# Optimization experiments

Hardware: AMD Instinct MI355X
Metric: run time of the kernel (lower is better)

The kernel has to match this reference:

```python
import jax, jax.numpy as jnp
import numpy as np

N = 8192        # num_nodes (also num output classes per the module)
F_IN = 512      # num_features
H = 64          # gcn_dim
E = N * 64      # edges (avg_degree 64)


def setup_inputs() -> dict:
    key = jax.random.key(0)
    k_x, k_e, k_w1, k_w2 = jax.random.split(key, 4)
    x = jax.random.normal(k_x, (N, F_IN), dtype=jnp.float32)
    edge_index = jax.random.randint(k_e, (2, E), 0, N, dtype=jnp.int64)
    # Glorot-ish init for the two GCN layer weights
    W1 = jax.random.normal(k_w1, (F_IN, H), dtype=jnp.float32) * (1.0 / np.sqrt(F_IN))
    b1 = jnp.zeros((H,), dtype=jnp.float32)
    W2 = jax.random.normal(k_w2, (H, N), dtype=jnp.float32) * (1.0 / np.sqrt(H))
    b2 = jnp.zeros((N,), dtype=jnp.float32)
    return {"x": x, "edge_index": edge_index, "W1": W1, "b1": b1, "W2": W2, "b2": b2}


def _gcn_conv(x, edge_index, W, b):
    """GCNConv: out = D^{-1/2} (A + I) D^{-1/2} (x @ W) + b."""
    n = x.shape[0]
    loops = jnp.arange(n, dtype=edge_index.dtype)
    src = jnp.concatenate([edge_index[0], loops])  # message source nodes
    dst = jnp.concatenate([edge_index[1], loops])  # aggregation targets
    deg = jax.ops.segment_sum(jnp.ones_like(dst, dtype=x.dtype), dst, num_segments=n)
    dinv = jnp.where(deg > 0, jax.lax.rsqrt(deg), 0.0)
    norm = dinv[src] * dinv[dst]                   # [E+n]
    xw = x @ W                                     # transform first (smaller msgs when W shrinks dim)
    msgs = xw[src] * norm[:, None]                 # gather + scale
    return jax.ops.segment_sum(msgs, dst, num_segments=n) + b


def reference(x, edge_index, W1, b1, W2, b2):
    h = jax.nn.relu(_gcn_conv(x, edge_index, W1, b1))   # [N, H]
    logits = _gcn_conv(h, edge_index, W2, b2)           # [N, N]
    return jax.nn.log_softmax(logits, axis=1)
```

## Files before the change

kernel.cpp:

```cpp
#include <hip/hip_runtime.h>
#include <hip/hip_bf16.h>

typedef __attribute__((ext_vector_type(8))) short short8;
typedef __attribute__((ext_vector_type(16))) float f32x16;
typedef __attribute__((ext_vector_type(4))) float f32x4;

#define NN 8192
#define FIN 512
#define HD 64
#define LOG2E 1.44269504088896f

#if __has_builtin(__builtin_amdgcn_exp2f)
#define EXP2(x) __builtin_amdgcn_exp2f(x)
#else
#define EXP2(x) exp2f(x)
#endif

__global__ void k_pack_zero(const float* __restrict__ W2, __hip_bfloat16* __restrict__ w2p,
                            int* __restrict__ cnt) {
    int i = blockIdx.x * blockDim.x + threadIdx.x;
    if (i < NN) cnt[i] = 0;
    int k  = i >> 13;
    int cc = i & 8191;
    int c32 = cc >> 5, cl = cc & 31;
    int kc = k >> 4, hh = (k >> 3) & 1, j = k & 7;
    int dsti = ((c32 * 4 + kc) * 64 + hh * 32 + cl) * 8 + j;
    w2p[dsti] = __float2bfloat16(W2[i]);
}

__global__ void k_count(const int* __restrict__ dst, int E, int* __restrict__ cnt) {
    int e = blockIdx.x * blockDim.x + threadIdx.x;
    if (e < E) atomicAdd(&cnt[dst[e]], 1);
}

__global__ __launch_bounds__(1024) void k_scan(const int* __restrict__ cnt,
        int* __restrict__ offs, int* __restrict__ cursor, float* __restrict__ dinv) {
    __shared__ int wsh[16];
    int t = threadIdx.x;
    int lane = t & 63, wv = t >> 6;
    int v[8], loc[8];
    int s = 0;
#pragma unroll
    for (int j = 0; j < 8; ++j) { v[j] = cnt[t*8+j]; loc[j] = s; s += v[j]; }
    int inc = s;
#pragma unroll
    for (int d = 1; d < 64; d <<= 1) {
        int up = __shfl_up(inc, d, 64);
        if (lane >= d) inc += up;
    }
    if (lane == 63) wsh[wv] = inc;
    __syncthreads();
    if (t < 16) {
        int mv = wsh[t];
        int winc = mv;
#pragma unroll
        for (int d = 1; d < 16; d <<= 1) {
            int up = __shfl_up(winc, d, 16);
            if (t >= d) winc += up;
        }
        wsh[t] = winc - mv;
    }
    __syncthreads();
    int base = wsh[wv] + (inc - s);
#pragma unroll
    for (int j = 0; j < 8; ++j) {
        int o = base + loc[j];
        offs[t*8+j]   = o;
        cursor[t*8+j] = o;
        dinv[t*8+j]   = rsqrtf((float)(v[j] + 1));
    }
    if (t == 1023) offs[NN] = base + s;
}

__global__ void k_scatter(const int* __restrict__ src, const int* __restrict__ dst, int E,
        int* __restrict__ cursor, int* __restrict__ ssrc) {
    int e = blockIdx.x * blockDim.x + threadIdx.x;
    if (e < E) {
        int pos = atomicAdd(&cursor[dst[e]], 1);
        ssrc[pos] = src[e];
    }
}

__global__ __launch_bounds__(256) void k_gemm1(const float* __restrict__ x,
        const float* __restrict__ W1, const float* __restrict__ dinv,
        float* __restrict__ xws) {
    __shared__ alignas(16) float Xs[16][132];
    int t = threadIdx.x;
    int c  = t & 63;
    int rg = t >> 6;
    int br = blockIdx.x * 16;
    float acc[4] = {0.f, 0.f, 0.f, 0.f};
    for (int k0 = 0; k0 < FIN; k0 += 128) {
        __syncthreads();
        int row_ld = t >> 4, kcol = (t & 15) * 8;
        const float* xp = x + (br + row_ld) * FIN + k0 + kcol;
        float4 v0 = *(const float4*)xp;
        float4 v1 = *(const float4*)(xp + 4);
        *(float4*)&Xs[row_ld][kcol]     = v0;
        *(float4*)&Xs[row_ld][kcol + 4] = v1;
        __syncthreads();
        int rg4 = rg * 4;
#pragma unroll 4
        for (int kk = 0; kk < 128; kk += 4) {
            f32x4 x0 = *(const f32x4*)&Xs[rg4 + 0][kk];
            f32x4 x1 = *(const f32x4*)&Xs[rg4 + 1][kk];
            f32x4 x2 = *(const f32x4*)&Xs[rg4 + 2][kk];
            f32x4 x3 = *(const f32x4*)&Xs[rg4 + 3][kk];
#pragma unroll
            for (int q = 0; q < 4; ++q) {
                float w = W1[(k0 + kk + q) * HD + c];
                acc[0] += x0[q] * w;
                acc[1] += x1[q] * w;
                acc[2] += x2[q] * w;
                acc[3] += x3[q] * w;
            }
        }
    }
#pragma unroll
    for (int r = 0; r < 4; ++r) {
        int row = br + rg*4 + r;
        xws[row * HD + c] = acc[r] * dinv[row];
    }
}

__global__ __launch_bounds__(256) void k_agg1(const float* __restrict__ xws,
        const int* __restrict__ offs, const int* __restrict__ ssrc,
        const float* __restrict__ dinv, const float* __restrict__ b1,
        float* __restrict__ hs) {
    int lane = threadIdx.x & 63;
    int node = (blockIdx.x << 2) + (threadIdx.x >> 6);
    const float* xp = xws + lane;
    float acc = xp[node * HD];
    int beg = offs[node], end = offs[node + 1];
    for (int base = beg; base < end; base += 64) {
        int rem = end - base;
        int n = rem < 64 ? rem : 64;
        int idx = (lane < n) ? ssrc[base + lane] : 0;
        int j = 0;
        for (; j + 8 <= n; j += 8) {
            int s0 = __shfl(idx, j+0, 64), s1 = __shfl(idx, j+1, 64);
            int s2 = __shfl(idx, j+2, 64), s3 = __shfl(idx, j+3, 64);
            int s4 = __shfl(idx, j+4, 64), s5 = __shfl(idx, j+5, 64);
            int s6 = __shfl(idx, j+6, 64), s7 = __shfl(idx, j+7, 64);
            float v0 = xp[s0*HD], v1 = xp[s1*HD], v2 = xp[s2*HD], v3 = xp[s3*HD];
            float v4 = xp[s4*HD], v5 = xp[s5*HD], v6 = xp[s6*HD], v7 = xp[s7*HD];
            acc += ((v0+v1)+(v2+v3)) + ((v4+v5)+(v6+v7));
        }
        for (; j < n; ++j) {
            int s = __shfl(idx, j, 64);
            acc += xp[s*HD];
        }
    }
    float dv = dinv[node];
    float h = fmaxf(acc * dv + b1[lane], 0.f);
    hs[node * HD + lane] = h * dv;
}

__global__ __launch_bounds__(256) void k_agg2(const float* __restrict__ hs,
        const int* __restrict__ offs, const int* __restrict__ ssrc,
        const float* __restrict__ dinv, __hip_bfloat16* __restrict__ gbf) {
    int lane = threadIdx.x & 63;
    int node = (blockIdx.x << 2) + (threadIdx.x >> 6);
    const float* hp = hs + lane;
    float acc = hp[node * HD];
    int beg = offs[node], end = offs[node + 1];
    for (int base = beg; base < end; base += 64) {
        int rem = end - base;
        int n = rem < 64 ? rem : 64;
        int idx = (lane < n) ? ssrc[base + lane] : 0;
        int j = 0;
        for (; j + 8 <= n; j += 8) {
            int s0 = __shfl(idx, j+0, 64), s1 = __shfl(idx, j+1, 64);
            int s2 = __shfl(idx, j+2, 64), s3 = __shfl(idx, j+3, 64);
            int s4 = __shfl(idx, j+4, 64), s5 = __shfl(idx, j+5, 64);
            int s6 = __shfl(idx, j+6, 64), s7 = __shfl(idx, j+7, 64);
            float v0 = hp[s0*HD], v1 = hp[s1*HD], v2 = hp[s2*HD], v3 = hp[s3*HD];
            float v4 = hp[s4*HD], v5 = hp[s5*HD], v6 = hp[s6*HD], v7 = hp[s7*HD];
            acc += ((v0+v1)+(v2+v3)) + ((v4+v5)+(v6+v7));
        }
        for (; j < n; ++j) {
            int s = __shfl(idx, j, 64);
            acc += hp[s*HD];
        }
    }
    gbf[node * HD + lane] = __float2bfloat16(acc * dinv[node]);
}

__global__ __launch_bounds__(512) void k_fused(
        const __hip_bfloat16* __restrict__ gbf,
        const __hip_bfloat16* __restrict__ w2p,
        const float* __restrict__ b2,
        float* __restrict__ out) {
    __shared__ float red[32][8];
    __shared__ float Lsh[32];
    const unsigned short* g  = (const unsigned short*)gbf;
    const unsigned short* wp = (const unsigned short*)w2p;
    int t = threadIdx.x;
    int lane = t & 63, wv = t >> 6;
    int cl = lane & 31, hh = lane >> 5;
    int row0 = blockIdx.x * 32;

    short8 a[4];
#pragma unroll
    for (int kc = 0; kc < 4; ++kc)
        a[kc] = *(const short8*)(g + (row0 + cl) * HD + kc*16 + hh*8);

    float sm[16];
#pragma unroll
    for (int r = 0; r < 16; ++r) sm[r] = 0.f;

    for (int it = 0; it < 32; ++it) {
        int c32 = wv * 32 + it;
        const unsigned short* bp = wp + c32 * 2048 + lane * 8;
        float bias = b2[c32 * 32 + cl];
        f32x16 d;
#pragma unroll
        for (int r = 0; r < 16; ++r) d[r] = 0.f;
#pragma unroll
        for (int kc = 0; kc < 4; ++kc) {
            short8 b = *(const short8*)(bp + kc * 512);
            d = __builtin_amdgcn_mfma_f32_32x32x16_bf16(a[kc], b, d, 0, 0, 0);
        }
#pragma unroll
        for (int r = 0; r < 16; ++r)
            sm[r] += EXP2((d[r] + bias) * LOG2E);
    }
#pragma unroll
    for (int r = 0; r < 16; ++r) {
#pragma unroll
        for (int msk = 1; msk < 32; msk <<= 1)
            sm[r] += __shfl_xor(sm[r], msk, 64);
    }
    if (cl == 0) {
#pragma unroll
        for (int r = 0; r < 16; ++r)
            red[(r & 3) + 8 * (r >> 2) + 4 * hh][wv] = sm[r];
    }
    __syncthreads();
    if (t < 32) {
        float s = 0.f;
#pragma unroll
        for (int j = 0; j < 8; ++j) s += red[t][j];
        Lsh[t] = logf(s);
    }
    __syncthreads();
    float L[16];
#pragma unroll
    for (int r = 0; r < 16; ++r)
        L[r] = Lsh[(r & 3) + 8 * (r >> 2) + 4 * hh];

    for (int it = 0; it < 32; ++it) {
        int c32 = wv * 32 + it;
        const unsigned short* bp = wp + c32 * 2048 + lane * 8;
        float bias = b2[c32 * 32 + cl];
        f32x16 d;
#pragma unroll
        for (int r = 0; r < 16; ++r) d[r] = 0.f;
#pragma unroll
        for (int kc = 0; kc < 4; ++kc) {
            short8 b = *(const short8*)(bp + kc * 512);
            d = __builtin_amdgcn_mfma_f32_32x32x16_bf16(a[kc], b, d, 0, 0, 0);
        }
        float* op = out + (size_t)row0 * NN + c32 * 32 + cl;
#pragma unroll
        for (int r = 0; r < 16; ++r) {
            int rp = (r & 3) + 8 * (r >> 2) + 4 * hh;
            __builtin_nontemporal_store(d[r] + bias - L[r], op + (size_t)rp * NN);
        }
    }
}

__global__ __launch_bounds__(512) void k_fused2(
        const float* __restrict__ hs,
        const int* __restrict__ offs, const int* __restrict__ ssrc,
        const float* __restrict__ dinv,
        const __hip_bfloat16* __restrict__ w2p,
        const float* __restrict__ b2,
        float* __restrict__ out) {
    __shared__ alignas(16) unsigned short gsh[32][72];
    __shared__ float red[32][8];
    __shared__ float Lsh[32];
    const unsigned short* wp = (const unsigned short*)w2p;
    int t = threadIdx.x;
    int lane = t & 63, wv = t >> 6;
    int cl = lane & 31, hh = lane >> 5;
    int row0 = blockIdx.x * 32;

    const float* hp = hs + lane;
    for (int q = 0; q < 4; ++q) {
        int r = wv * 4 + q;
        int node = row0 + r;
        float acc = hp[node * HD];
        int beg = offs[node], end = offs[node + 1];
        for (int base = beg; base < end; base += 64) {
            int rem = end - base;
            int n = rem < 64 ? rem : 64;
            int idx = (lane < n) ? ssrc[base + lane] : 0;
            int j = 0;
            for (; j + 8 <= n; j += 8) {
                int s0 = __shfl(idx, j+0, 64), s1 = __shfl(idx, j+1, 64);
                int s2 = __shfl(idx, j+2, 64), s3 = __shfl(idx, j+3, 64);
                int s4 = __shfl(idx, j+4, 64), s5 = __shfl(idx, j+5, 64);
                int s6 = __shfl(idx, j+6, 64), s7 = __shfl(idx, j+7, 64);
                float v0 = hp[s0*HD], v1 = hp[s1*HD], v2 = hp[s2*HD], v3 = hp[s3*HD];
                float v4 = hp[s4*HD], v5 = hp[s5*HD], v6 = hp[s6*HD], v7 = hp[s7*HD];
                acc += ((v0+v1)+(v2+v3)) + ((v4+v5)+(v6+v7));
            }
            for (; j < n; ++j) {
                int s = __shfl(idx, j, 64);
                acc += hp[s*HD];
            }
        }
        __hip_bfloat16 hv = __float2bfloat16(acc * dinv[node]);
        gsh[r][lane] = *reinterpret_cast<unsigned short*>(&hv);
    }
    __syncthreads();

    short8 a[4];
#pragma unroll
    for (int kc = 0; kc < 4; ++kc)
        a[kc] = *(const short8*)&gsh[cl][kc * 16 + hh * 8];

    const unsigned short* bpw = wp + (wv * 32) * 2048 + lane * 8;
    const float* bias_c = b2 + wv * 1024 + cl;

    float sm[16];
#pragma unroll
    for (int r = 0; r < 16; ++r) sm[r] = 0.f;

    short8 bc[4];
#pragma unroll
    for (int kc = 0; kc < 4; ++kc) bc[kc] = *(const short8*)(bpw + kc * 512);
    for (int it = 0; it < 32; ++it) {
        int itn = (it + 1) & 31;
        const unsigned short* bq = bpw + itn * 2048;
        short8 bn[4];
#pragma unroll
        for (int kc = 0; kc < 4; ++kc) bn[kc] = *(const short8*)(bq + kc * 512);
        float bias = bias_c[it * 32];
        f32x16 d;
#pragma unroll
        for (int r = 0; r < 16; ++r) d[r] = 0.f;
#pragma unroll
        for (int kc = 0; kc < 4; ++kc)
            d = __builtin_amdgcn_mfma_f32_32x32x16_bf16(a[kc], bc[kc], d, 0, 0, 0);
#pragma unroll
        for (int r = 0; r < 16; ++r)
            sm[r] += EXP2((d[r] + bias) * LOG2E);
#pragma unroll
        for (int kc = 0; kc < 4; ++kc) bc[kc] = bn[kc];
    }
#pragma unroll
    for (int r = 0; r < 16; ++r) {
#pragma unroll
        for (int msk = 1; msk < 32; msk <<= 1)
            sm[r] += __shfl_xor(sm[r], msk, 64);
    }
    if (cl == 0) {
#pragma unroll
        for (int r = 0; r < 16; ++r)
            red[(r & 3) + 8 * (r >> 2) + 4 * hh][wv] = sm[r];
    }
    __syncthreads();
    if (t < 32) {
        float s = 0.f;
#pragma unroll
        for (int j = 0; j < 8; ++j) s += red[t][j];
        Lsh[t] = logf(s);
    }
    __syncthreads();
    float L[16];
#pragma unroll
    for (int r = 0; r < 16; ++r)
        L[r] = Lsh[(r & 3) + 8 * (r >> 2) + 4 * hh];

#pragma unroll
    for (int kc = 0; kc < 4; ++kc) bc[kc] = *(const short8*)(bpw + kc * 512);
    for (int it = 0; it < 32; ++it) {
        int itn = (it + 1) & 31;
        const unsigned short* bq = bpw + itn * 2048;
        short8 bn[4];
#pragma unroll
        for (int kc = 0; kc < 4; ++kc) bn[kc] = *(const short8*)(bq + kc * 512);
        int c32 = wv * 32 + it;
        float bias = bias_c[it * 32];
        f32x16 d;
#pragma unroll
        for (int r = 0; r < 16; ++r) d[r] = 0.f;
#pragma unroll
        for (int kc = 0; kc < 4; ++kc)
            d = __builtin_amdgcn_mfma_f32_32x32x16_bf16(a[kc], bc[kc], d, 0, 0, 0);
        float* op = out + (size_t)row0 * NN + c32 * 32 + cl;
#pragma unroll
        for (int r = 0; r < 16; ++r) {
            int rp = (r & 3) + 8 * (r >> 2) + 4 * hh;
            __builtin_nontemporal_store(d[r] + bias - L[r], op + (size_t)rp * NN);
        }
#pragma unroll
        for (int kc = 0; kc < 4; ++kc) bc[kc] = bn[kc];
    }
}

extern "C" void kernel_launch(void* const* d_in, const int* in_sizes, int n_in,
                              void* d_out, int out_size, void* d_ws, size_t ws_size,
                              hipStream_t stream) {
    const float* x  = (const float*)d_in[0];
    const int*   ei = (const int*)d_in[1];
    const float* W1 = (const float*)d_in[2];
    const float* b1 = (const float*)d_in[3];
    const float* W2 = (const float*)d_in[4];
    const float* b2 = (const float*)d_in[5];
    float* out = (float*)d_out;
    int E = in_sizes[1] / 2;
    const int* esrc = ei;
    const int* edst = ei + E;

    char* w = (char*)d_ws;
    int*   cnt    = (int*)(w);
    int*   offs   = (int*)(w + (32 << 10));
    int*   cursor = (int*)(w + (68 << 10));
    float* dinv   = (float*)(w + (100 << 10));
    __hip_bfloat16* w2p = (__hip_bfloat16*)(w + (192 << 10));

    size_t total = (size_t)NN * NN;
    size_t need_fused = (size_t)(192 << 10) + (1 << 20) + (size_t)NN * HD * sizeof(float);
    bool fused_path = ws_size >= need_fused;

    int eb = (E + 255) / 256;
    k_pack_zero<<<(HD * NN) / 256, 256, 0, stream>>>(W2, w2p, cnt);
    k_count  <<<eb, 256, 0, stream>>>(edst, E, cnt);
    k_scan   <<<1, 1024, 0, stream>>>(cnt, offs, cursor, dinv);

    if (fused_path) {
        float* hs   = (float*)(w + (192 << 10) + (1 << 20));
        float* xws  = out + total - (size_t)NN * HD;
        int*   ssrc = (int*)xws - E;
        k_scatter<<<eb, 256, 0, stream>>>(esrc, edst, E, cursor, ssrc);
        k_gemm1  <<<NN / 16, 256, 0, stream>>>(x, W1, dinv, xws);
        k_agg1   <<<NN / 4, 256, 0, stream>>>(xws, offs, ssrc, dinv, b1, hs);
        k_fused2 <<<NN / 32, 512, 0, stream>>>(hs, offs, ssrc, dinv, w2p, b2, out);
    } else {
        __hip_bfloat16* gbf = (__hip_bfloat16*)(w + (192 << 10) + (1 << 20));
        float* hs   = out + total - (size_t)NN * HD;
        float* xws  = hs  - (size_t)NN * HD;
        int*   ssrc = (int*)xws - E;
        k_scatter<<<eb, 256, 0, stream>>>(esrc, edst, E, cursor, ssrc);
        k_gemm1  <<<NN / 16, 256, 0, stream>>>(x, W1, dinv, xws);
        k_agg1   <<<NN / 4, 256, 0, stream>>>(xws, offs, ssrc, dinv, b1, hs);
        k_agg2   <<<NN / 4, 256, 0, stream>>>(hs, offs, ssrc, dinv, gbf);
        k_fused  <<<NN / 32, 512, 0, stream>>>(gbf, w2p, b2, out);
    }
}
```

Measured before the change: 437.7 us.

## Merge edge scatter into gemm1 launch and vectorize pack, count, scan accesses

The edge scatter and the first GEMM are merged into one launch, with extra blocks doing the scatter, so the two independent stages can overlap and one launch is removed. The W2 bf16 pack now has each thread gather eight strided values and write one 16-byte vector instead of scattering single elements. Edge counting and scattering read four indices per thread through int4 loads, and the scan uses vector loads and stores. The risks are uncoalesced strided reads in the pack, and int4 loads that depend on the edge arrays being 16-byte aligned.

```diff
diff --git a/kernel.cpp b/kernel.cpp
--- a/kernel.cpp
+++ b/kernel.cpp
@@ -20,17 +20,32 @@
                             int* __restrict__ cnt) {
     int i = blockIdx.x * blockDim.x + threadIdx.x;
     if (i < NN) cnt[i] = 0;
-    int k  = i >> 13;
-    int cc = i & 8191;
-    int c32 = cc >> 5, cl = cc & 31;
-    int kc = k >> 4, hh = (k >> 3) & 1, j = k & 7;
-    int dsti = ((c32 * 4 + kc) * 64 + hh * 32 + cl) * 8 + j;
-    w2p[dsti] = __float2bfloat16(W2[i]);
+    int cl  = i & 31;
+    int hh  = (i >> 5) & 1;
+    int kc  = (i >> 6) & 3;
+    int c32 = i >> 8;
+    const float* wsrc = W2 + (size_t)(kc * 16 + hh * 8) * NN + c32 * 32 + cl;
+    union { short8 v; unsigned short u[8]; } ov;
+#pragma unroll
+    for (int j = 0; j < 8; ++j) {
+        __hip_bfloat16 hv = __float2bfloat16(wsrc[(size_t)j * NN]);
+        ov.u[j] = *reinterpret_cast<unsigned short*>(&hv);
+    }
+    ((short8*)w2p)[i] = ov.v;
 }
 
 __global__ void k_count(const int* __restrict__ dst, int E, int* __restrict__ cnt) {
-    int e = blockIdx.x * blockDim.x + threadIdx.x;
-    if (e < E) atomicAdd(&cnt[dst[e]], 1);
+    int e4 = blockIdx.x * blockDim.x + threadIdx.x;
+    int e = e4 * 4;
+    if (e + 3 < E) {
+        int4 d = ((const int4*)dst)[e4];
+        atomicAdd(&cnt[d.x], 1);
+        atomicAdd(&cnt[d.y], 1);
+        atomicAdd(&cnt[d.z], 1);
+        atomicAdd(&cnt[d.w], 1);
+    } else {
+        for (int q = e; q < E; ++q) atomicAdd(&cnt[dst[q]], 1);
+    }
 }
 
 __global__ __launch_bounds__(1024) void k_scan(const int* __restrict__ cnt,
@@ -38,10 +53,13 @@
     __shared__ int wsh[16];
     int t = threadIdx.x;
     int lane = t & 63, wv = t >> 6;
-    int v[8], loc[8];
+    int4 va = ((const int4*)cnt)[t * 2];
+    int4 vb = ((const int4*)cnt)[t * 2 + 1];
+    int v[8] = {va.x, va.y, va.z, va.w, vb.x, vb.y, vb.z, vb.w};
+    int loc[8];
     int s = 0;
 #pragma unroll
-    for (int j = 0; j < 8; ++j) { v[j] = cnt[t*8+j]; loc[j] = s; s += v[j]; }
+    for (int j = 0; j < 8; ++j) { loc[j] = s; s += v[j]; }
     int inc = s;
 #pragma unroll
     for (int d = 1; d < 64; d <<= 1) {
@@ -62,30 +80,46 @@
     }
     __syncthreads();
     int base = wsh[wv] + (inc - s);
-#pragma unroll
-    for (int j = 0; j < 8; ++j) {
-        int o = base + loc[j];
-        offs[t*8+j]   = o;
-        cursor[t*8+j] = o;
-        dinv[t*8+j]   = rsqrtf((float)(v[j] + 1));
-    }
+    int4 oa = {base + loc[0], base + loc[1], base + loc[2], base + loc[3]};
+    int4 ob = {base + loc[4], base + loc[5], base + loc[6], base + loc[7]};
+    ((int4*)offs)[t * 2]     = oa;
+    ((int4*)offs)[t * 2 + 1] = ob;
+    ((int4*)cursor)[t * 2]     = oa;
+    ((int4*)cursor)[t * 2 + 1] = ob;
+    float4 da = {rsqrtf((float)(v[0] + 1)), rsqrtf((float)(v[1] + 1)),
+                 rsqrtf((float)(v[2] + 1)), rsqrtf((float)(v[3] + 1))};
+    float4 db = {rsqrtf((float)(v[4] + 1)), rsqrtf((float)(v[5] + 1)),
+                 rsqrtf((float)(v[6] + 1)), rsqrtf((float)(v[7] + 1))};
+    ((float4*)dinv)[t * 2]     = da;
+    ((float4*)dinv)[t * 2 + 1] = db;
     if (t == 1023) offs[NN] = base + s;
 }
 
-__global__ void k_scatter(const int* __restrict__ src, const int* __restrict__ dst, int E,
+__global__ __launch_bounds__(256) void k_mid(const float* __restrict__ x,
+        const float* __restrict__ W1, const float* __restrict__ dinv,
+        float* __restrict__ xws,
+        const int* __restrict__ src, const int* __restrict__ dst, int E,
         int* __restrict__ cursor, int* __restrict__ ssrc) {
-    int e = blockIdx.x * blockDim.x + threadIdx.x;
-    if (e < E) {
-        int pos = atomicAdd(&cursor[dst[e]], 1);
-        ssrc[pos] = src[e];
-    }
-}
-
-__global__ __launch_bounds__(256) void k_gemm1(const float* __restrict__ x,
-        const float* __restrict__ W1, const float* __restrict__ dinv,
-        float* __restrict__ xws) {
     __shared__ alignas(16) float Xs[16][132];
     int t = threadIdx.x;
+    if (blockIdx.x >= NN / 16) {
+        int e4 = (blockIdx.x - NN / 16) * 256 + t;
+        int e = e4 * 4;
+        if (e + 3 < E) {
+            int4 d = ((const int4*)dst)[e4];
+            int4 sv = ((const int4*)src)[e4];
+            int p0 = atomicAdd(&cursor[d.x], 1); ssrc[p0] = sv.x;
+            int p1 = atomicAdd(&cursor[d.y], 1); ssrc[p1] = sv.y;
+            int p2 = atomicAdd(&cursor[d.z], 1); ssrc[p2] = sv.z;
+            int p3 = atomicAdd(&cursor[d.w], 1); ssrc[p3] = sv.w;
+        } else {
+            for (int q = e; q < E; ++q) {
+                int pos = atomicAdd(&cursor[dst[q]], 1);
+                ssrc[pos] = src[q];
+            }
+        }
+        return;
+    }
     int c  = t & 63;
     int rg = t >> 6;
     int br = blockIdx.x * 16;
@@ -426,17 +460,18 @@
     size_t need_fused = (size_t)(192 << 10) + (1 << 20) + (size_t)NN * HD * sizeof(float);
     bool fused_path = ws_size >= need_fused;
 
-    int eb = (E + 255) / 256;
-    k_pack_zero<<<(HD * NN) / 256, 256, 0, stream>>>(W2, w2p, cnt);
-    k_count  <<<eb, 256, 0, stream>>>(edst, E, cnt);
+    int cb = ((E + 3) / 4 + 255) / 256;
+    int gb = NN / 16;
+
+    k_pack_zero<<<(HD * NN / 8) / 256, 256, 0, stream>>>(W2, w2p, cnt);
+    k_count  <<<cb, 256, 0, stream>>>(edst, E, cnt);
     k_scan   <<<1, 1024, 0, stream>>>(cnt, offs, cursor, dinv);
 
     if (fused_path) {
         float* hs   = (float*)(w + (192 << 10) + (1 << 20));
         float* xws  = out + total - (size_t)NN * HD;
         int*   ssrc = (int*)xws - E;
-        k_scatter<<<eb, 256, 0, stream>>>(esrc, edst, E, cursor, ssrc);
-        k_gemm1  <<<NN / 16, 256, 0, stream>>>(x, W1, dinv, xws);
+        k_mid    <<<gb + cb, 256, 0, stream>>>(x, W1, dinv, xws, esrc, edst, E, cursor, ssrc);
         k_agg1   <<<NN / 4, 256, 0, stream>>>(xws, offs, ssrc, dinv, b1, hs);
         k_fused2 <<<NN / 32, 512, 0, stream>>>(hs, offs, ssrc, dinv, w2p, b2, out);
     } else {
@@ -444,8 +479,7 @@
         float* hs   = out + total - (size_t)NN * HD;
         float* xws  = hs  - (size_t)NN * HD;
         int*   ssrc = (int*)xws - E;
-        k_scatter<<<eb, 256, 0, stream>>>(esrc, edst, E, cursor, ssrc);
-        k_gemm1  <<<NN / 16, 256, 0, stream>>>(x, W1, dinv, xws);
+        k_mid    <<<gb + cb, 256, 0, stream>>>(x, W1, dinv, xws, esrc, edst, E, cursor, ssrc);
         k_agg1   <<<NN / 4, 256, 0, stream>>>(xws, offs, ssrc, dinv, b1, hs);
         k_agg2   <<<NN / 4, 256, 0, stream>>>(hs, offs, ssrc, dinv, gbf);
         k_fused  <<<NN / 32, 512, 0, stream>>>(gbf, w2p, b2, out);
```

New measurement: 428.9 us. -2.0%, faster.
